# Performance work log

Measured on AMD Instinct MI355X. Metric: run time of the kernel, lower is better.

The kernel has to match this reference:

```python
import jax, jax.numpy as jnp
import numpy as np

B = 256          # batch
NUM_CAPS = 10    # output capsules
NUM_ROUTE = 1152 # route nodes (e.g., 32*6*6 primary capsules)
IN_CH = 8        # input capsule dim
OUT_CH = 16      # output capsule dim
NUM_ITER = 3     # routing iterations


def setup_inputs() -> dict:
    key = jax.random.key(0)
    k1, k2 = jax.random.split(key)
    x = jax.random.normal(k1, (B, NUM_ROUTE, IN_CH), dtype=jnp.float32)
    route_weights = jax.random.normal(k2, (NUM_CAPS, NUM_ROUTE, IN_CH, OUT_CH), dtype=jnp.float32)
    return {"x": x, "route_weights": route_weights}


def squash(t, axis=-1):
    sq = jnp.sum(t * t, axis=axis, keepdims=True)
    return (sq / (1.0 + sq)) * t / jnp.sqrt(sq)


def reference(x, route_weights):
    # priors: x[:,None,:,None,:] @ W[None] -> [B, NC, NR, 1, OC]
    priors = jnp.einsum('bri,crio->bcro', x, route_weights)[:, :, :, None, :]
    logits = jnp.zeros_like(priors)  # zeros(*priors.size())
    outputs = None
    for i in range(NUM_ITER):
        # original softmaxes over dim=2 (route-node axis)
        probs = jax.nn.softmax(logits, axis=2)
        outputs = squash(jnp.sum(probs * priors, axis=2, keepdims=True))  # [B,NC,1,1,OC]
        if i != NUM_ITER - 1:
            # delta_logits: [B,NC,NR,1,1], broadcast-added to full-shape logits
            logits = logits + jnp.sum(priors * outputs, axis=-1, keepdims=True)
    return outputs
```

## Files before the change

### kernel.cpp

```cpp
#include <hip/hip_runtime.h>
#include <math.h>


#define NBATCH 256
#define NC 10
#define NR 1152
#define IC 8
#define OC 16
#define NITER 3
#define T 512
#define MB 2
#define RPT 9

__device__ __forceinline__ float wave_sum(float v) {
#pragma unroll
    for (int m = 1; m <= 32; m <<= 1) v += __shfl_xor(v, m, 64);
    return v;
}
__device__ __forceinline__ float wave_max(float v) {
#pragma unroll
    for (int m = 1; m <= 32; m <<= 1) v = fmaxf(v, __shfl_xor(v, m, 64));
    return v;
}

__global__ __launch_bounds__(T)
__attribute__((amdgpu_waves_per_eu(4, 4)))
void caps_route(
    const float* __restrict__ x,
    const float* __restrict__ W,
    float* __restrict__ out)
{
    __shared__ float smem[NR * 16];
    __shared__ float red[2 * 128];
    __shared__ float vout[2 * OC];

    const int t    = threadIdx.x;
    const int og   = t & 3;
    const int rr   = t >> 2;
    const int lane = t & 63;
    const int wid  = t >> 6;

    const int c  = blockIdx.x >> 7;
    const int bp = blockIdx.x & 127;
    const int b0 = bp * 2;

    float4* xs4 = (float4*)smem;
    const float4* __restrict__ xg = (const float4*)(x + (size_t)b0 * (NR * IC));
    for (int k = t; k < NR * 4; k += T) xs4[k] = xg[k];
    __syncthreads();

    float4 pri0[RPT], pri1[RPT];
    const float4* __restrict__ wb = (const float4*)(W + (size_t)c * (NR * IC * OC));
    const float4* xb0 = xs4;
    const float4* xb1 = xs4 + NR * 2;
#pragma unroll
    for (int p = 0; p < RPT; ++p) {
        const int r = rr + (p << 7);
        float4 xa0 = xb0[2 * r], xc0 = xb0[2 * r + 1];
        float4 xa1 = xb1[2 * r], xc1 = xb1[2 * r + 1];
        float xv0[8] = {xa0.x, xa0.y, xa0.z, xa0.w, xc0.x, xc0.y, xc0.z, xc0.w};
        float xv1[8] = {xa1.x, xa1.y, xa1.z, xa1.w, xc1.x, xc1.y, xc1.z, xc1.w};
        const float4* wp = wb + (size_t)r * 32 + og;
        float4 a0 = make_float4(0.f, 0.f, 0.f, 0.f);
        float4 a1 = make_float4(0.f, 0.f, 0.f, 0.f);
#pragma unroll
        for (int i = 0; i < 8; ++i) {
            float4 w = wp[i * 4];
            a0.x = fmaf(xv0[i], w.x, a0.x); a1.x = fmaf(xv1[i], w.x, a1.x);
            a0.y = fmaf(xv0[i], w.y, a0.y); a1.y = fmaf(xv1[i], w.y, a1.y);
            a0.z = fmaf(xv0[i], w.z, a0.z); a1.z = fmaf(xv1[i], w.z, a1.z);
            a0.w = fmaf(xv0[i], w.w, a0.w); a1.w = fmaf(xv1[i], w.w, a1.w);
        }
        pri0[p] = a0;
        pri1[p] = a1;
    }
    float* logit0 = smem;
    float* logit1 = smem + NR;

    for (int it = 0; it < NITER; ++it) {
        const bool uni = (it == 0);
        float m0 = 0.f, m1 = 0.f, invd0 = 0.f, invd1 = 0.f;
        if (!uni) {
            float lm0 = -3.4e38f, lm1 = -3.4e38f;
#pragma unroll
            for (int k = 0; k < 3; ++k) {
                int r = t + (k << 9);
                if (r < NR) {
                    lm0 = fmaxf(lm0, logit0[r]);
                    lm1 = fmaxf(lm1, logit1[r]);
                }
            }
            lm0 = wave_max(lm0); lm1 = wave_max(lm1);
            if (lane == 0) { red[wid] = lm0; red[16 + wid] = lm1; }
            __syncthreads();
            m0 = red[0]; m1 = red[16];
#pragma unroll
            for (int w = 1; w < 8; ++w) {
                m0 = fmaxf(m0, red[w]); m1 = fmaxf(m1, red[16 + w]);
            }
            float ls0 = 0.f, ls1 = 0.f;
#pragma unroll
            for (int k = 0; k < 3; ++k) {
                int r = t + (k << 9);
                if (r < NR) {
                    ls0 += __expf(logit0[r] - m0);
                    ls1 += __expf(logit1[r] - m1);
                }
            }
            ls0 = wave_sum(ls0); ls1 = wave_sum(ls1);
            __syncthreads();
            if (lane == 0) { red[wid] = ls0; red[16 + wid] = ls1; }
            __syncthreads();
            float d0 = red[0], d1 = red[16];
#pragma unroll
            for (int w = 1; w < 8; ++w) { d0 += red[w]; d1 += red[16 + w]; }
            invd0 = 1.f / d0; invd1 = 1.f / d1;
        }

        float4 s0 = make_float4(0.f, 0.f, 0.f, 0.f);
        float4 s1 = make_float4(0.f, 0.f, 0.f, 0.f);
#pragma unroll
        for (int k = 0; k < RPT; ++k) {
            float w0 = 1.0f, w1 = 1.0f;
            if (!uni) {
                const int r = rr + (k << 7);
                w0 = __expf(logit0[r] - m0);
                w1 = __expf(logit1[r] - m1);
            }
            s0.x = fmaf(w0, pri0[k].x, s0.x); s1.x = fmaf(w1, pri1[k].x, s1.x);
            s0.y = fmaf(w0, pri0[k].y, s0.y); s1.y = fmaf(w1, pri1[k].y, s1.y);
            s0.z = fmaf(w0, pri0[k].z, s0.z); s1.z = fmaf(w1, pri1[k].z, s1.z);
            s0.w = fmaf(w0, pri0[k].w, s0.w); s1.w = fmaf(w1, pri1[k].w, s1.w);
        }
#pragma unroll
        for (int msk = 4; msk <= 32; msk <<= 1) {
            s0.x += __shfl_xor(s0.x, msk, 64); s1.x += __shfl_xor(s1.x, msk, 64);
            s0.y += __shfl_xor(s0.y, msk, 64); s1.y += __shfl_xor(s1.y, msk, 64);
            s0.z += __shfl_xor(s0.z, msk, 64); s1.z += __shfl_xor(s1.z, msk, 64);
            s0.w += __shfl_xor(s0.w, msk, 64); s1.w += __shfl_xor(s1.w, msk, 64);
        }
        __syncthreads();
        if (lane < 4) {
            ((float4*)red)[wid * 4 + og]         = s0;
            ((float4*)(red + 128))[wid * 4 + og] = s1;
        }
        __syncthreads();

        if (t < 2 * OC) {
            const int bsel = t >> 4, o = t & 15;
            float s = 0.f;
#pragma unroll
            for (int w = 0; w < 8; ++w) s += red[bsel * 128 + w * 16 + o];
            s *= uni ? (1.0f / 1152.0f) : (bsel ? invd1 : invd0);
            float sq = s * s;
#pragma unroll
            for (int msk = 1; msk <= 8; msk <<= 1) sq += __shfl_xor(sq, msk, 64);
            float v = s * (sqrtf(sq) / (1.0f + sq));
            if (it == NITER - 1) out[((size_t)(b0 + bsel) * NC + c) * OC + o] = v;
            else vout[t] = v;
        }
        __syncthreads();

        if (it < NITER - 1) {
            float4 v0 = ((const float4*)vout)[og];
            float4 v1 = ((const float4*)(vout + OC))[og];
#pragma unroll
            for (int k = 0; k < RPT; ++k) {
                const int r = rr + (k << 7);
                float d0 = pri0[k].x * v0.x + pri0[k].y * v0.y +
                           pri0[k].z * v0.z + pri0[k].w * v0.w;
                float d1 = pri1[k].x * v1.x + pri1[k].y * v1.y +
                           pri1[k].z * v1.z + pri1[k].w * v1.w;
                d0 += __shfl_xor(d0, 1, 64); d1 += __shfl_xor(d1, 1, 64);
                d0 += __shfl_xor(d0, 2, 64); d1 += __shfl_xor(d1, 2, 64);
                if (og == 0) {
                    if (it == 0) { logit0[r] = d0; logit1[r] = d1; }
                    else         { logit0[r] += d0; logit1[r] += d1; }
                }
            }
            __syncthreads();
        }
    }
}

extern "C" void kernel_launch(void* const* d_in, const int* in_sizes, int n_in,
                              void* d_out, int out_size, void* d_ws, size_t ws_size,
                              hipStream_t stream) {
    const float* x = (const float*)d_in[0];
    const float* W = (const float*)d_in[1];
    float* out = (float*)d_out;
    caps_route<<<dim3(NC * (NBATCH / MB)), dim3(T), 0, stream>>>(x, W, out);
}
```

Baseline: 131.7 us.

## Process one batch per block, drop x staging in shared memory

Each block now handles a single batch element instead of two, reads x directly from global memory instead of staging it in LDS, and shrinks shared memory to just the logits. The per-thread prior registers are halved, and the waves-per-EU hint is raised to allow higher occupancy. In exchange, each W tile is reused across only one batch element, so W global/L2 traffic doubles, and twice as many blocks are launched, each with the same fixed reduction and synchronisation overhead.

```diff
diff --git a/kernel.cpp b/kernel.cpp
--- a/kernel.cpp
+++ b/kernel.cpp
@@ -9,7 +9,6 @@
 #define OC 16
 #define NITER 3
 #define T 512
-#define MB 2
 #define RPT 9
 
 __device__ __forceinline__ float wave_sum(float v) {
@@ -24,15 +23,15 @@
 }
 
 __global__ __launch_bounds__(T)
-__attribute__((amdgpu_waves_per_eu(4, 4)))
+__attribute__((amdgpu_waves_per_eu(6)))
 void caps_route(
     const float* __restrict__ x,
     const float* __restrict__ W,
     float* __restrict__ out)
 {
-    __shared__ float smem[NR * 16];
-    __shared__ float red[2 * 128];
-    __shared__ float vout[2 * OC];
+    __shared__ float logit[NR];
+    __shared__ float red[128];
+    __shared__ float vout[OC];
 
     const int t    = threadIdx.x;
     const int og   = t & 3;
@@ -40,142 +39,109 @@
     const int lane = t & 63;
     const int wid  = t >> 6;
 
-    const int c  = blockIdx.x >> 7;
-    const int bp = blockIdx.x & 127;
-    const int b0 = bp * 2;
+    const int c = blockIdx.x >> 8;
+    const int b = blockIdx.x & 255;
 
-    float4* xs4 = (float4*)smem;
-    const float4* __restrict__ xg = (const float4*)(x + (size_t)b0 * (NR * IC));
-    for (int k = t; k < NR * 4; k += T) xs4[k] = xg[k];
-    __syncthreads();
-
-    float4 pri0[RPT], pri1[RPT];
+    float4 pri[RPT];
     const float4* __restrict__ wb = (const float4*)(W + (size_t)c * (NR * IC * OC));
-    const float4* xb0 = xs4;
-    const float4* xb1 = xs4 + NR * 2;
+    const float4* __restrict__ xg = (const float4*)(x + (size_t)b * (NR * IC));
 #pragma unroll
     for (int p = 0; p < RPT; ++p) {
         const int r = rr + (p << 7);
-        float4 xa0 = xb0[2 * r], xc0 = xb0[2 * r + 1];
-        float4 xa1 = xb1[2 * r], xc1 = xb1[2 * r + 1];
-        float xv0[8] = {xa0.x, xa0.y, xa0.z, xa0.w, xc0.x, xc0.y, xc0.z, xc0.w};
-        float xv1[8] = {xa1.x, xa1.y, xa1.z, xa1.w, xc1.x, xc1.y, xc1.z, xc1.w};
+        float4 xa = xg[2 * r], xc = xg[2 * r + 1];
+        float xv[8] = {xa.x, xa.y, xa.z, xa.w, xc.x, xc.y, xc.z, xc.w};
         const float4* wp = wb + (size_t)r * 32 + og;
-        float4 a0 = make_float4(0.f, 0.f, 0.f, 0.f);
-        float4 a1 = make_float4(0.f, 0.f, 0.f, 0.f);
+        float4 a = make_float4(0.f, 0.f, 0.f, 0.f);
 #pragma unroll
         for (int i = 0; i < 8; ++i) {
             float4 w = wp[i * 4];
-            a0.x = fmaf(xv0[i], w.x, a0.x); a1.x = fmaf(xv1[i], w.x, a1.x);
-            a0.y = fmaf(xv0[i], w.y, a0.y); a1.y = fmaf(xv1[i], w.y, a1.y);
-            a0.z = fmaf(xv0[i], w.z, a0.z); a1.z = fmaf(xv1[i], w.z, a1.z);
-            a0.w = fmaf(xv0[i], w.w, a0.w); a1.w = fmaf(xv1[i], w.w, a1.w);
+            a.x = fmaf(xv[i], w.x, a.x);
+            a.y = fmaf(xv[i], w.y, a.y);
+            a.z = fmaf(xv[i], w.z, a.z);
+            a.w = fmaf(xv[i], w.w, a.w);
         }
-        pri0[p] = a0;
-        pri1[p] = a1;
+        pri[p] = a;
     }
-    float* logit0 = smem;
-    float* logit1 = smem + NR;
 
     for (int it = 0; it < NITER; ++it) {
         const bool uni = (it == 0);
-        float m0 = 0.f, m1 = 0.f, invd0 = 0.f, invd1 = 0.f;
+        float m = 0.f, invd = 0.f;
         if (!uni) {
-            float lm0 = -3.4e38f, lm1 = -3.4e38f;
+            float lm = -3.4e38f;
 #pragma unroll
             for (int k = 0; k < 3; ++k) {
                 int r = t + (k << 9);
-                if (r < NR) {
-                    lm0 = fmaxf(lm0, logit0[r]);
-                    lm1 = fmaxf(lm1, logit1[r]);
-                }
+                if (r < NR) lm = fmaxf(lm, logit[r]);
             }
-            lm0 = wave_max(lm0); lm1 = wave_max(lm1);
-            if (lane == 0) { red[wid] = lm0; red[16 + wid] = lm1; }
+            lm = wave_max(lm);
+            if (lane == 0) red[wid] = lm;
             __syncthreads();
-            m0 = red[0]; m1 = red[16];
+            m = red[0];
 #pragma unroll
-            for (int w = 1; w < 8; ++w) {
-                m0 = fmaxf(m0, red[w]); m1 = fmaxf(m1, red[16 + w]);
-            }
-            float ls0 = 0.f, ls1 = 0.f;
+            for (int w = 1; w < 8; ++w) m = fmaxf(m, red[w]);
+            float ls = 0.f;
 #pragma unroll
             for (int k = 0; k < 3; ++k) {
                 int r = t + (k << 9);
-                if (r < NR) {
-                    ls0 += __expf(logit0[r] - m0);
-                    ls1 += __expf(logit1[r] - m1);
-                }
+                if (r < NR) ls += __expf(logit[r] - m);
             }
-            ls0 = wave_sum(ls0); ls1 = wave_sum(ls1);
+            ls = wave_sum(ls);
             __syncthreads();
-            if (lane == 0) { red[wid] = ls0; red[16 + wid] = ls1; }
+            if (lane == 0) red[wid] = ls;
             __syncthreads();
-            float d0 = red[0], d1 = red[16];
+            float d = red[0];
 #pragma unroll
-            for (int w = 1; w < 8; ++w) { d0 += red[w]; d1 += red[16 + w]; }
-            invd0 = 1.f / d0; invd1 = 1.f / d1;
+            for (int w = 1; w < 8; ++w) d += red[w];
+            invd = 1.f / d;
         }
 
-        float4 s0 = make_float4(0.f, 0.f, 0.f, 0.f);
-        float4 s1 = make_float4(0.f, 0.f, 0.f, 0.f);
+        float4 s = make_float4(0.f, 0.f, 0.f, 0.f);
 #pragma unroll
         for (int k = 0; k < RPT; ++k) {
-            float w0 = 1.0f, w1 = 1.0f;
-            if (!uni) {
-                const int r = rr + (k << 7);
-                w0 = __expf(logit0[r] - m0);
-                w1 = __expf(logit1[r] - m1);
-            }
-            s0.x = fmaf(w0, pri0[k].x, s0.x); s1.x = fmaf(w1, pri1[k].x, s1.x);
-            s0.y = fmaf(w0, pri0[k].y, s0.y); s1.y = fmaf(w1, pri1[k].y, s1.y);
-            s0.z = fmaf(w0, pri0[k].z, s0.z); s1.z = fmaf(w1, pri1[k].z, s1.z);
-            s0.w = fmaf(w0, pri0[k].w, s0.w); s1.w = fmaf(w1, pri1[k].w, s1.w);
+            float w = 1.0f;
+            if (!uni) w = __expf(logit[rr + (k << 7)] - m);
+            s.x = fmaf(w, pri[k].x, s.x);
+            s.y = fmaf(w, pri[k].y, s.y);
+            s.z = fmaf(w, pri[k].z, s.z);
+            s.w = fmaf(w, pri[k].w, s.w);
         }
 #pragma unroll
         for (int msk = 4; msk <= 32; msk <<= 1) {
-            s0.x += __shfl_xor(s0.x, msk, 64); s1.x += __shfl_xor(s1.x, msk, 64);
-            s0.y += __shfl_xor(s0.y, msk, 64); s1.y += __shfl_xor(s1.y, msk, 64);
-            s0.z += __shfl_xor(s0.z, msk, 64); s1.z += __shfl_xor(s1.z, msk, 64);
-            s0.w += __shfl_xor(s0.w, msk, 64); s1.w += __shfl_xor(s1.w, msk, 64);
+            s.x += __shfl_xor(s.x, msk, 64);
+            s.y += __shfl_xor(s.y, msk, 64);
+            s.z += __shfl_xor(s.z, msk, 64);
+            s.w += __shfl_xor(s.w, msk, 64);
         }
         __syncthreads();
-        if (lane < 4) {
-            ((float4*)red)[wid * 4 + og]         = s0;
-            ((float4*)(red + 128))[wid * 4 + og] = s1;
-        }
+        if (lane < 4) ((float4*)red)[wid * 4 + og] = s;
         __syncthreads();
 
-        if (t < 2 * OC) {
-            const int bsel = t >> 4, o = t & 15;
-            float s = 0.f;
+        if (t < OC) {
+            float sv = 0.f;
 #pragma unroll
-            for (int w = 0; w < 8; ++w) s += red[bsel * 128 + w * 16 + o];
-            s *= uni ? (1.0f / 1152.0f) : (bsel ? invd1 : invd0);
-            float sq = s * s;
+            for (int w = 0; w < 8; ++w) sv += red[w * 16 + t];
+            sv *= uni ? (1.0f / 1152.0f) : invd;
+            float sq = sv * sv;
 #pragma unroll
             for (int msk = 1; msk <= 8; msk <<= 1) sq += __shfl_xor(sq, msk, 64);
-            float v = s * (sqrtf(sq) / (1.0f + sq));
-            if (it == NITER - 1) out[((size_t)(b0 + bsel) * NC + c) * OC + o] = v;
+            float v = sv * (sqrtf(sq) / (1.0f + sq));
+            if (it == NITER - 1) out[((size_t)b * NC + c) * OC + t] = v;
             else vout[t] = v;
         }
         __syncthreads();
 
         if (it < NITER - 1) {
-            float4 v0 = ((const float4*)vout)[og];
-            float4 v1 = ((const float4*)(vout + OC))[og];
+            float4 v4 = ((const float4*)vout)[og];
 #pragma unroll
             for (int k = 0; k < RPT; ++k) {
                 const int r = rr + (k << 7);
-                float d0 = pri0[k].x * v0.x + pri0[k].y * v0.y +
-                           pri0[k].z * v0.z + pri0[k].w * v0.w;
-                float d1 = pri1[k].x * v1.x + pri1[k].y * v1.y +
-                           pri1[k].z * v1.z + pri1[k].w * v1.w;
-                d0 += __shfl_xor(d0, 1, 64); d1 += __shfl_xor(d1, 1, 64);
-                d0 += __shfl_xor(d0, 2, 64); d1 += __shfl_xor(d1, 2, 64);
+                float d = pri[k].x * v4.x + pri[k].y * v4.y +
+                          pri[k].z * v4.z + pri[k].w * v4.w;
+                d += __shfl_xor(d, 1, 64);
+                d += __shfl_xor(d, 2, 64);
                 if (og == 0) {
-                    if (it == 0) { logit0[r] = d0; logit1[r] = d1; }
-                    else         { logit0[r] += d0; logit1[r] += d1; }
+                    if (it == 0) logit[r] = d;
+                    else         logit[r] += d;
                 }
             }
             __syncthreads();
@@ -189,5 +155,5 @@
     const float* x = (const float*)d_in[0];
     const float* W = (const float*)d_in[1];
     float* out = (float*)d_out;
-    caps_route<<<dim3(NC * (NBATCH / MB)), dim3(T), 0, stream>>>(x, W, out);
+    caps_route<<<dim3(NC * NBATCH), dim3(T), 0, stream>>>(x, W, out);
 }
```

Measured after the change: 139.0 us. 5.6% more time.

## Repack route weights into thread-coalesced layout and drop x shared-memory staging

Applied to the files above, without the earlier changes.

Adds a pre-pass kernel that reorders the route weights into the workspace so that each thread's float4 loads during the priors computation are contiguous across the block. The main kernel no longer copies x into shared memory; it reads x directly from global memory, which shrinks LDS use to the logit arrays and the occupancy hint is raised from 4 to 5 waves per EU. The trade is an extra launch and a full read and write of W on every call, plus uncached global x reads. The old layout is kept as a fallback when the workspace is too small.

```diff
diff --git a/kernel.cpp b/kernel.cpp
--- a/kernel.cpp
+++ b/kernel.cpp
@@ -11,6 +11,19 @@
 #define T 512
 #define MB 2
 #define RPT 9
+#define WP_F4 (NC * RPT * 8 * T)
+
+__global__ __launch_bounds__(256)
+void repack_w(const float4* __restrict__ W4, float4* __restrict__ Wp) {
+    int j = blockIdx.x * 256 + threadIdx.x;
+    int t  = j & 511;
+    int pk = (j >> 9) % 72;
+    int c  = (j >> 9) / 72;
+    int p  = pk >> 3, k = pk & 7;
+    int r  = (t >> 2) + (p << 7);
+    int og = t & 3;
+    Wp[j] = W4[(((size_t)c * NR + r) * IC + k) * 4 + og];
+}
 
 __device__ __forceinline__ float wave_sum(float v) {
 #pragma unroll
@@ -23,14 +36,16 @@
     return v;
 }
 
+template <bool PACKED>
 __global__ __launch_bounds__(T)
-__attribute__((amdgpu_waves_per_eu(4, 4)))
+__attribute__((amdgpu_waves_per_eu(5, 5)))
 void caps_route(
     const float* __restrict__ x,
-    const float* __restrict__ W,
+    const float4* __restrict__ Wg,
     float* __restrict__ out)
 {
-    __shared__ float smem[NR * 16];
+    __shared__ float logit0[NR];
+    __shared__ float logit1[NR];
     __shared__ float red[2 * 128];
     __shared__ float vout[2 * OC];
 
@@ -44,38 +59,56 @@
     const int bp = blockIdx.x & 127;
     const int b0 = bp * 2;
 
-    float4* xs4 = (float4*)smem;
-    const float4* __restrict__ xg = (const float4*)(x + (size_t)b0 * (NR * IC));
-    for (int k = t; k < NR * 4; k += T) xs4[k] = xg[k];
-    __syncthreads();
-
     float4 pri0[RPT], pri1[RPT];
-    const float4* __restrict__ wb = (const float4*)(W + (size_t)c * (NR * IC * OC));
-    const float4* xb0 = xs4;
-    const float4* xb1 = xs4 + NR * 2;
-#pragma unroll
-    for (int p = 0; p < RPT; ++p) {
-        const int r = rr + (p << 7);
-        float4 xa0 = xb0[2 * r], xc0 = xb0[2 * r + 1];
-        float4 xa1 = xb1[2 * r], xc1 = xb1[2 * r + 1];
-        float xv0[8] = {xa0.x, xa0.y, xa0.z, xa0.w, xc0.x, xc0.y, xc0.z, xc0.w};
-        float xv1[8] = {xa1.x, xa1.y, xa1.z, xa1.w, xc1.x, xc1.y, xc1.z, xc1.w};
-        const float4* wp = wb + (size_t)r * 32 + og;
-        float4 a0 = make_float4(0.f, 0.f, 0.f, 0.f);
-        float4 a1 = make_float4(0.f, 0.f, 0.f, 0.f);
-#pragma unroll
-        for (int i = 0; i < 8; ++i) {
-            float4 w = wp[i * 4];
-            a0.x = fmaf(xv0[i], w.x, a0.x); a1.x = fmaf(xv1[i], w.x, a1.x);
-            a0.y = fmaf(xv0[i], w.y, a0.y); a1.y = fmaf(xv1[i], w.y, a1.y);
-            a0.z = fmaf(xv0[i], w.z, a0.z); a1.z = fmaf(xv1[i], w.z, a1.z);
-            a0.w = fmaf(xv0[i], w.w, a0.w); a1.w = fmaf(xv1[i], w.w, a1.w);
-        }
-        pri0[p] = a0;
-        pri1[p] = a1;
+    const float4* __restrict__ xg0 = (const float4*)(x + (size_t)b0 * (NR * IC));
+    const float4* __restrict__ xg1 = xg0 + NR * 2;
+
+    if (PACKED) {
+        const float4* __restrict__ wp = Wg + (size_t)c * (RPT * 8 * T) + t;
+#pragma unroll
+        for (int p = 0; p < RPT; ++p) {
+            const int r = rr + (p << 7);
+            float4 xa0 = xg0[2 * r], xc0 = xg0[2 * r + 1];
+            float4 xa1 = xg1[2 * r], xc1 = xg1[2 * r + 1];
+            float xv0[8] = {xa0.x, xa0.y, xa0.z, xa0.w, xc0.x, xc0.y, xc0.z, xc0.w};
+            float xv1[8] = {xa1.x, xa1.y, xa1.z, xa1.w, xc1.x, xc1.y, xc1.z, xc1.w};
+            float4 a0 = make_float4(0.f, 0.f, 0.f, 0.f);
+            float4 a1 = make_float4(0.f, 0.f, 0.f, 0.f);
+#pragma unroll
+            for (int k = 0; k < 8; ++k) {
+                float4 w = wp[(p * 8 + k) * T];
+                a0.x = fmaf(xv0[k], w.x, a0.x); a1.x = fmaf(xv1[k], w.x, a1.x);
+                a0.y = fmaf(xv0[k], w.y, a0.y); a1.y = fmaf(xv1[k], w.y, a1.y);
+                a0.z = fmaf(xv0[k], w.z, a0.z); a1.z = fmaf(xv1[k], w.z, a1.z);
+                a0.w = fmaf(xv0[k], w.w, a0.w); a1.w = fmaf(xv1[k], w.w, a1.w);
+            }
+            pri0[p] = a0;
+            pri1[p] = a1;
+        }
+    } else {
+        const float4* __restrict__ wb = Wg + (size_t)c * (NR * IC * 4);
+#pragma unroll
+        for (int p = 0; p < RPT; ++p) {
+            const int r = rr + (p << 7);
+            float4 xa0 = xg0[2 * r], xc0 = xg0[2 * r + 1];
+            float4 xa1 = xg1[2 * r], xc1 = xg1[2 * r + 1];
+            float xv0[8] = {xa0.x, xa0.y, xa0.z, xa0.w, xc0.x, xc0.y, xc0.z, xc0.w};
+            float xv1[8] = {xa1.x, xa1.y, xa1.z, xa1.w, xc1.x, xc1.y, xc1.z, xc1.w};
+            const float4* wp = wb + (size_t)r * 32 + og;
+            float4 a0 = make_float4(0.f, 0.f, 0.f, 0.f);
+            float4 a1 = make_float4(0.f, 0.f, 0.f, 0.f);
+#pragma unroll
+            for (int k = 0; k < 8; ++k) {
+                float4 w = wp[k * 4];
+                a0.x = fmaf(xv0[k], w.x, a0.x); a1.x = fmaf(xv1[k], w.x, a1.x);
+                a0.y = fmaf(xv0[k], w.y, a0.y); a1.y = fmaf(xv1[k], w.y, a1.y);
+                a0.z = fmaf(xv0[k], w.z, a0.z); a1.z = fmaf(xv1[k], w.z, a1.z);
+                a0.w = fmaf(xv0[k], w.w, a0.w); a1.w = fmaf(xv1[k], w.w, a1.w);
+            }
+            pri0[p] = a0;
+            pri1[p] = a1;
+        }
     }
-    float* logit0 = smem;
-    float* logit1 = smem + NR;
 
     for (int it = 0; it < NITER; ++it) {
         const bool uni = (it == 0);
@@ -189,5 +222,14 @@
     const float* x = (const float*)d_in[0];
     const float* W = (const float*)d_in[1];
     float* out = (float*)d_out;
-    caps_route<<<dim3(NC * (NBATCH / MB)), dim3(T), 0, stream>>>(x, W, out);
-}
+    const size_t wp_bytes = (size_t)WP_F4 * sizeof(float4);
+    if (d_ws != nullptr && ws_size >= wp_bytes) {
+        repack_w<<<dim3(WP_F4 / 256), dim3(256), 0, stream>>>(
+            (const float4*)W, (float4*)d_ws);
+        caps_route<true><<<dim3(NC * (NBATCH / MB)), dim3(T), 0, stream>>>(
+            x, (const float4*)d_ws, out);
+    } else {
+        caps_route<false><<<dim3(NC * (NBATCH / MB)), dim3(T), 0, stream>>>(
+            x, (const float4*)W, out);
+    }
+}
```

After: 169.2 us. 1.28x slower.
